# Optimization experiments

Measured on AMD Instinct MI355X. Metric: run time of the kernel, lower is better.

## Reference

```python
import jax, jax.numpy as jnp
import numpy as np

B, LC, LP = 8, 1024, 512
D, H, F, V, NL = 512, 8, 2048, 70, 4
MAXLEN = 2048
HD = D // H
EPS = 1e-5


def setup_inputs() -> dict:
    key = jax.random.key(0)
    ks = iter(jax.random.split(key, 64))
    s = lambda *sh: jax.random.normal(next(ks), sh, jnp.float32) * 0.02
    inp = {}
    inp['cds'] = jax.random.randint(next(ks), (B, LC), 0, V)
    inp['enc_prot'] = jax.random.normal(next(ks), (B, LP, D), jnp.float32)
    causal = jnp.tril(jnp.ones((LC, LC), jnp.int32))
    inp['cds_mask'] = jnp.broadcast_to(causal[None, None], (B, 1, LC, LC))
    inp['prot_mask'] = jnp.ones((B, 1, 1, LP), jnp.int32)
    inp['tok_emb'] = s(V, D)
    inp['pos_emb'] = s(MAXLEN, D)
    for p in ['sa', 'ca']:
        for m in ['q', 'k', 'v', 'o']:
            inp[f'{p}_w{m}'] = s(NL, D, D)
            inp[f'{p}_b{m}'] = jnp.zeros((NL, D), jnp.float32)
    inp['ff_w1'] = s(NL, D, F)
    inp['ff_b1'] = jnp.zeros((NL, F), jnp.float32)
    inp['ff_w2'] = s(NL, F, D)
    inp['ff_b2'] = jnp.zeros((NL, D), jnp.float32)
    for i in [1, 2, 3]:
        inp[f'ln{i}_g'] = jnp.ones((NL, D), jnp.float32)
        inp[f'ln{i}_b'] = jnp.zeros((NL, D), jnp.float32)
    inp['fc_out_w'] = s(D, V)
    inp['fc_out_b'] = jnp.zeros((V,), jnp.float32)
    return inp


def layernorm(x, g, b):
    mu = jnp.mean(x, -1, keepdims=True)
    var = jnp.var(x, -1, keepdims=True)
    return (x - mu) * jax.lax.rsqrt(var + EPS) * g + b


def mha(q_in, k_in, v_in, wq, bq, wk, bk, wv, bv, wo, bo, mask):
    b, lq, _ = q_in.shape
    lk = k_in.shape[1]
    q = (q_in @ wq + bq).reshape(b, lq, H, HD).transpose(0, 2, 1, 3)
    k = (k_in @ wk + bk).reshape(b, lk, H, HD).transpose(0, 2, 1, 3)
    v = (v_in @ wv + bv).reshape(b, lk, H, HD).transpose(0, 2, 1, 3)
    scores = jnp.einsum('bhqd,bhkd->bhqk', q, k) / jnp.sqrt(jnp.float32(HD))
    scores = jnp.where(mask == 0, -jnp.inf, scores)
    attn = jax.nn.softmax(scores, axis=-1)
    out = jnp.einsum('bhqk,bhkd->bhqd', attn, v)
    out = out.transpose(0, 2, 1, 3).reshape(b, lq, D)
    return out @ wo + bo, attn


def reference(cds, enc_prot, cds_mask, prot_mask, tok_emb, pos_emb,
              sa_wq, sa_bq, sa_wk, sa_bk, sa_wv, sa_bv, sa_wo, sa_bo,
              ca_wq, ca_bq, ca_wk, ca_bk, ca_wv, ca_bv, ca_wo, ca_bo,
              ff_w1, ff_b1, ff_w2, ff_b2,
              ln1_g, ln1_b, ln2_g, ln2_b, ln3_g, ln3_b,
              fc_out_w, fc_out_b):
    lc = cds.shape[1]
    x = tok_emb[cds] * jnp.sqrt(jnp.float32(D)) + pos_emb[:lc][None]
    attn = None
    for i in range(NL):
        sa, _ = mha(x, x, x, sa_wq[i], sa_bq[i], sa_wk[i], sa_bk[i],
                    sa_wv[i], sa_bv[i], sa_wo[i], sa_bo[i], cds_mask)
        x = layernorm(x + sa, ln1_g[i], ln1_b[i])
        ca, attn = mha(x, enc_prot, enc_prot, ca_wq[i], ca_bq[i], ca_wk[i], ca_bk[i],
                       ca_wv[i], ca_bv[i], ca_wo[i], ca_bo[i], prot_mask)
        x = layernorm(x + ca, ln2_g[i], ln2_b[i])
        ff = jax.nn.relu(x @ ff_w1[i] + ff_b1[i]) @ ff_w2[i] + ff_b2[i]
        x = layernorm(x + ff, ln3_g[i], ln3_b[i])
    logits = x @ fc_out_w + fc_out_b
    return logits, attn
```

## Files before the change

### kernel.cpp

```cpp
#include <hip/hip_runtime.h>

typedef __attribute__((ext_vector_type(8))) short bf16x8;
typedef __attribute__((ext_vector_type(4))) short bf16x4;
typedef __attribute__((ext_vector_type(4))) float f32x4;

#define D_MODEL 512
#define N_HEADS 8
#define HEAD_DIM 64
#define SEQ_C 1024
#define SEQ_P 512
#define BATCH 8
#define FFDIM 2048
#define VOCAB 70
#define NLAYER 4
#define MQ (BATCH*SEQ_C)
#define MKV (BATCH*SEQ_P)
#define KSTR 72

__device__ __forceinline__ short f2bs(float f) {
  union { float f; unsigned u; } v; v.f = f;
  unsigned r = (v.u + 0x7FFFu + ((v.u >> 16) & 1u)) >> 16;
  return (short)r;
}

__device__ __forceinline__ void gl_lds16(const void* g, void* l) {
  __builtin_amdgcn_global_load_lds(
      (const __attribute__((address_space(1))) void*)g,
      (__attribute__((address_space(3))) void*)l, 16, 0, 0);
}

__global__ __launch_bounds__(256)
void embed_kernel(const int* __restrict__ cds, const float* __restrict__ tok,
                  const float* __restrict__ pos, float* __restrict__ x,
                  short* __restrict__ xb) {
  int idx = blockIdx.x * 256 + threadIdx.x;
  int row = idx >> 9, c = idx & 511;
  int l = row & (SEQ_C - 1);
  int t = cds[row];
  float v = tok[t * D_MODEL + c] * 22.627416997969522f + pos[l * D_MODEL + c];
  x[idx] = v;
  xb[idx] = f2bs(v);
}

__global__ __launch_bounds__(256)
void cvtf2b_kernel(const float* __restrict__ in, short* __restrict__ out) {
  int i = (blockIdx.x * 256 + threadIdx.x) * 4;
  float4 v = *(const float4*)(in + i);
  bf16x4 o;
  o[0] = f2bs(v.x); o[1] = f2bs(v.y); o[2] = f2bs(v.z); o[3] = f2bs(v.w);
  *(bf16x4*)(out + i) = o;
}

struct WtArgs {
  const float* src[8];
  short* dst[8];
  size_t ldz[8];
  int row_off[8];
};

__global__ __launch_bounds__(256)
void wtrans8_kernel(WtArgs a) {
  __shared__ float T[32][33];
  int z = blockIdx.z;
  int job = z >> 2, layer = z & 3;
  const float* W = a.src[job] + (size_t)layer * D_MODEL * D_MODEL;
  short* Wt = a.dst[job] + (size_t)layer * a.ldz[job];
  int row_off = a.row_off[job];
  int n0 = blockIdx.x * 32, k0 = blockIdx.y * 32;
  int r = threadIdx.x >> 3, c4 = (threadIdx.x & 7) * 4;
  float4 v = *(const float4*)(W + (size_t)(k0 + r) * D_MODEL + n0 + c4);
  T[c4 + 0][r] = v.x; T[c4 + 1][r] = v.y; T[c4 + 2][r] = v.z; T[c4 + 3][r] = v.w;
  __syncthreads();
  bf16x4 o;
  o[0] = f2bs(T[r][c4 + 0]); o[1] = f2bs(T[r][c4 + 1]);
  o[2] = f2bs(T[r][c4 + 2]); o[3] = f2bs(T[r][c4 + 3]);
  *(bf16x4*)&Wt[(size_t)(row_off + n0 + r) * D_MODEL + k0 + c4] = o;
}

__global__ __launch_bounds__(256)
void wtrans_kernel(const float* __restrict__ W, short* __restrict__ Wt,
                   int K, int N, size_t dst_ldz) {
  __shared__ float T[32][33];
  size_t lo_s = (size_t)blockIdx.z * K * N;
  size_t lo_d = (size_t)blockIdx.z * dst_ldz;
  int n0 = blockIdx.x * 32, k0 = blockIdx.y * 32;
  int r = threadIdx.x >> 3, c4 = (threadIdx.x & 7) * 4;
  float4 v = *(const float4*)(W + lo_s + (size_t)(k0 + r) * N + n0 + c4);
  T[c4 + 0][r] = v.x; T[c4 + 1][r] = v.y; T[c4 + 2][r] = v.z; T[c4 + 3][r] = v.w;
  __syncthreads();
  bf16x4 o;
  o[0] = f2bs(T[r][c4 + 0]); o[1] = f2bs(T[r][c4 + 1]);
  o[2] = f2bs(T[r][c4 + 2]); o[3] = f2bs(T[r][c4 + 3]);
  *(bf16x4*)&Wt[lo_d + (size_t)(n0 + r) * K + k0 + c4] = o;
}

__global__ __launch_bounds__(256)
void logits_wt_kernel(const float* __restrict__ w, short* __restrict__ wt) {
  int idx = blockIdx.x * 256 + threadIdx.x;
  int r = idx >> 9, c = idx & 511;
  wt[idx] = (r < VOCAB) ? f2bs(w[c * VOCAB + r]) : (short)0;
}

template<int ACT, int OMODE, int MT>
__global__ __launch_bounds__(256)
void gemm_mfma(const short* __restrict__ Ab, const short* __restrict__ Wt,
               const float* __restrict__ b0, const float* __restrict__ b1,
               const float* __restrict__ b2,
               float* __restrict__ Cf, short* __restrict__ Cb,
               int N, int K, int ldc, size_t segstride) {
  constexpr int MREP = MT / 32;
  __shared__ __align__(16) short As[2][MT * 32];
  __shared__ __align__(16) short Bs[2][4096];
  int tid = threadIdx.x, lane = tid & 63, w = tid >> 6;
  int quad = lane >> 4, ln = lane & 15;
  int row0 = blockIdx.x * MT, col0 = blockIdx.y * 128;
  int q0 = tid, q1 = tid + 256;
  const short* a0 = Ab + (size_t)(row0 + (q0 >> 2)) * K + (q0 & 3) * 8;
  const short* a1 = Ab + (size_t)(row0 + (q1 >> 2)) * K + (q1 & 3) * 8;
  const short* w0 = Wt + (size_t)(col0 + (q0 >> 2)) * K + (q0 & 3) * 8;
  const short* w1 = Wt + (size_t)(col0 + (q1 >> 2)) * K + (q1 & 3) * 8;
  int wr = (w >> 1) * (MT / 2), wc = (w & 1) * 64;
  f32x4 acc[MREP][4];
  #pragma unroll
  for (int mb = 0; mb < MREP; mb++)
    #pragma unroll
    for (int nb = 0; nb < 4; nb++) acc[mb][nb] = (f32x4){0.f, 0.f, 0.f, 0.f};

  int nt = K >> 5;
#define STG(ko, buf) do { \
    gl_lds16(a0 + (ko), &As[buf][w * 512]); \
    if (MT == 128) gl_lds16(a1 + (ko), &As[buf][MT * 16 + w * 512]); \
    gl_lds16(w0 + (ko), &Bs[buf][w * 512]); \
    gl_lds16(w1 + (ko), &Bs[buf][2048 + w * 512]); } while (0)

  STG(0, 0);
  __syncthreads();
  for (int t = 0; t < nt; t++) {
    int cur = t & 1;
    if (t + 1 < nt) STG((t + 1) << 5, cur ^ 1);
    bf16x8 af[MREP], bfr[4];
    #pragma unroll
    for (int i = 0; i < MREP; i++)
      af[i] = *(const bf16x8*)&As[cur][(wr + i * 16 + ln) * 32 + quad * 8];
    #pragma unroll
    for (int i = 0; i < 4; i++)
      bfr[i] = *(const bf16x8*)&Bs[cur][(wc + i * 16 + ln) * 32 + quad * 8];
    #pragma unroll
    for (int mb = 0; mb < MREP; mb++)
      #pragma unroll
      for (int nb = 0; nb < 4; nb++)
        acc[mb][nb] = __builtin_amdgcn_mfma_f32_16x16x32_bf16(
            af[mb], bfr[nb], acc[mb][nb], 0, 0, 0);
    __syncthreads();
  }
#undef STG

  int colb = col0 + wc;
  const float* bp = b0;
  if (OMODE == 2) {
    int seg = colb >> 9;
    bp = (seg == 0) ? b0 : (seg == 1) ? b1 : b2;
  }
  float bv[4];
  #pragma unroll
  for (int nb = 0; nb < 4; nb++) {
    int col = colb + nb * 16 + ln;
    if (OMODE == 3)      bv[nb] = (col < ldc) ? bp[col] : 0.f;
    else if (OMODE == 2) bv[nb] = bp[col & 511];
    else                 bv[nb] = bp[col];
  }
  size_t segoff = (OMODE == 2) ? (size_t)(colb >> 9) * segstride : 0;
  #pragma unroll
  for (int mb = 0; mb < MREP; mb++)
    #pragma unroll
    for (int i = 0; i < 4; i++) {
      size_t r = (size_t)(row0 + wr + mb * 16 + quad * 4 + i);
      #pragma unroll
      for (int nb = 0; nb < 4; nb++) {
        int col = colb + nb * 16 + ln;
        float v = acc[mb][nb][i] + bv[nb];
        if (ACT) v = fmaxf(v, 0.f);
        if (OMODE == 0)      Cf[r * ldc + col] = v;
        else if (OMODE == 1) Cb[r * ldc + col] = f2bs(v);
        else if (OMODE == 2) Cb[segoff + r * 512 + (col & 511)] = f2bs(v);
        else if (col < ldc)  Cf[r * ldc + col] = v;
      }
    }
}

template<bool CAUSAL, bool SAVE_ML>
__global__ __launch_bounds__(256)
void flash_mfma(const short* __restrict__ Q, const short* __restrict__ K,
                const short* __restrict__ V, short* __restrict__ O,
                float* __restrict__ m_out, float* __restrict__ l_out,
                int LQ, int LK) {
  __shared__ short Ks[64 * KSTR];
  __shared__ short Vt[64 * KSTR];
  __shared__ short Ps[4 * 16 * KSTR];
  const float scale = 0.125f;
  int qt = CAUSAL ? ((int)gridDim.x - 1 - (int)blockIdx.x) : (int)blockIdx.x;
  int bh = blockIdx.y;
  int b = bh >> 3, h = bh & 7;
  int tid = threadIdx.x, lane = tid & 63, w = tid >> 6;
  int quad = lane >> 4, ln = lane & 15;

  const short* qp = Q + (size_t)(b * LQ + qt * 64 + w * 16 + ln) * D_MODEL + h * HEAD_DIM;
  bf16x8 qf[2];
  qf[0] = *(const bf16x8*)(qp + quad * 8);
  qf[1] = *(const bf16x8*)(qp + 32 + quad * 8);

  int qrow = qt * 64 + w * 16 + ln;
  float m_q = -__builtin_inff(), l_q = 0.f;
  f32x4 o_acc[4];
  #pragma unroll
  for (int nb = 0; nb < 4; nb++) o_acc[nb] = (f32x4){0.f, 0.f, 0.f, 0.f};

  const short* Kb = K + (size_t)(b * LK) * D_MODEL + h * HEAD_DIM;
  const short* Vb = V + (size_t)(b * LK) * D_MODEL + h * HEAD_DIM;
  int sr = tid >> 2, sc = (tid & 3) * 16;
  int br4 = (tid >> 4) * 4, bc4 = (tid & 15) * 4;

  bf16x8 krA, krB;
  bf16x4 vr0, vr1, vr2, vr3;

#define LOADKV(KT) do { \
    const short* kg_ = Kb + (size_t)((KT) * 64 + sr) * D_MODEL + sc; \
    krA = *(const bf16x8*)kg_; krB = *(const bf16x8*)(kg_ + 8); \
    const short* vg_ = Vb + (size_t)((KT) * 64 + br4) * D_MODEL + bc4; \
    vr0 = *(const bf16x4*)(vg_); \
    vr1 = *(const bf16x4*)(vg_ + D_MODEL); \
    vr2 = *(const bf16x4*)(vg_ + 2 * D_MODEL); \
    vr3 = *(const bf16x4*)(vg_ + 3 * D_MODEL); } while (0)

  LOADKV(0);
  int nkt = CAUSAL ? (qt + 1) : (LK >> 6);
  for (int kt = 0; kt < nkt; kt++) {
    __syncthreads();
    *(bf16x8*)&Ks[sr * KSTR + sc]     = krA;
    *(bf16x8*)&Ks[sr * KSTR + sc + 8] = krB;
    #pragma unroll
    for (int jj = 0; jj < 4; jj++) {
      bf16x4 t;
      t[0] = vr0[jj]; t[1] = vr1[jj]; t[2] = vr2[jj]; t[3] = vr3[jj];
      *(bf16x4*)&Vt[(bc4 + jj) * KSTR + br4] = t;
    }
    if (kt + 1 < nkt) LOADKV(kt + 1);
    __syncthreads();

    f32x4 st[4];
    __builtin_amdgcn_s_setprio(1);
    #pragma unroll
    for (int nb = 0; nb < 4; nb++) {
      st[nb] = (f32x4){0.f, 0.f, 0.f, 0.f};
      bf16x8 kf0 = *(const bf16x8*)&Ks[(nb * 16 + ln) * KSTR + quad * 8];
      bf16x8 kf1 = *(const bf16x8*)&Ks[(nb * 16 + ln) * KSTR + 32 + quad * 8];
      st[nb] = __builtin_amdgcn_mfma_f32_16x16x32_bf16(kf0, qf[0], st[nb], 0, 0, 0);
      st[nb] = __builtin_amdgcn_mfma_f32_16x16x32_bf16(kf1, qf[1], st[nb], 0, 0, 0);
    }
    __builtin_amdgcn_s_setprio(0);

    float sv[4][4];
    float mt = -__builtin_inff();
    #pragma unroll
    for (int nb = 0; nb < 4; nb++)
      #pragma unroll
      for (int i = 0; i < 4; i++) {
        float v = st[nb][i] * scale;
        if (CAUSAL && (kt * 64 + nb * 16 + quad * 4 + i) > qrow) v = -__builtin_inff();
        sv[nb][i] = v;
        mt = fmaxf(mt, v);
      }
    mt = fmaxf(mt, __shfl_xor(mt, 16));
    mt = fmaxf(mt, __shfl_xor(mt, 32));
    float mnew = fmaxf(m_q, mt);
    float alpha = __expf(m_q - mnew);
    float rs = 0.f;
    bf16x4 pk[4];
    #pragma unroll
    for (int nb = 0; nb < 4; nb++)
      #pragma unroll
      for (int i = 0; i < 4; i++) {
        float p = __expf(sv[nb][i] - mnew);
        rs += p;
        pk[nb][i] = f2bs(p);
      }
    rs += __shfl_xor(rs, 16);
    rs += __shfl_xor(rs, 32);
    l_q = l_q * alpha + rs;
    m_q = mnew;

    #pragma unroll
    for (int nb = 0; nb < 4; nb++)
      *(bf16x4*)&Ps[w * 16 * KSTR + ln * KSTR + nb * 16 + quad * 4] = pk[nb];
    #pragma unroll
    for (int i = 0; i < 4; i++) {
      float ai = __shfl(alpha, ((lane >> 4) << 2) + i);
      #pragma unroll
      for (int nb = 0; nb < 4; nb++) o_acc[nb][i] *= ai;
    }

    __builtin_amdgcn_s_setprio(1);
    #pragma unroll
    for (int kb = 0; kb < 2; kb++) {
      bf16x8 pf = *(const bf16x8*)&Ps[w * 16 * KSTR + ln * KSTR + kb * 32 + quad * 8];
      #pragma unroll
      for (int nb = 0; nb < 4; nb++) {
        bf16x8 vf = *(const bf16x8*)&Vt[(nb * 16 + ln) * KSTR + kb * 32 + quad * 8];
        o_acc[nb] = __builtin_amdgcn_mfma_f32_16x16x32_bf16(pf, vf, o_acc[nb], 0, 0, 0);
      }
    }
    __builtin_amdgcn_s_setprio(0);
  }
#undef LOADKV

  short* Ob = O + (size_t)(b * LQ + qt * 64 + w * 16 + quad * 4) * D_MODEL + h * HEAD_DIM;
  #pragma unroll
  for (int i = 0; i < 4; i++) {
    float li = __shfl(l_q, ((lane >> 4) << 2) + i);
    float inv = 1.f / li;
    #pragma unroll
    for (int nb = 0; nb < 4; nb++)
      Ob[(size_t)i * D_MODEL + nb * 16 + ln] = f2bs(o_acc[nb][i] * inv);
  }
  if (SAVE_ML && lane < 16) {
    int r = bh * LQ + qt * 64 + w * 16 + lane;
    m_out[r] = m_q;
    l_out[r] = l_q;
  }
}

__global__ __launch_bounds__(256)
void attn_prob_mfma(const short* __restrict__ Q, const short* __restrict__ K,
                    const float* __restrict__ m_in, const float* __restrict__ l_in,
                    float* __restrict__ out) {
  __shared__ short Ks[64 * KSTR];
  const float scale = 0.125f;
  int qt = blockIdx.x, bh = blockIdx.y;
  int b = bh >> 3, h = bh & 7;
  int tid = threadIdx.x, lane = tid & 63, w = tid >> 6;
  int quad = lane >> 4, ln = lane & 15;
  const short* qp = Q + (size_t)(b * SEQ_C + qt * 64 + w * 16 + ln) * D_MODEL + h * HEAD_DIM;
  bf16x8 qf[2];
  qf[0] = *(const bf16x8*)(qp + quad * 8);
  qf[1] = *(const bf16x8*)(qp + 32 + quad * 8);
  float m_r[4], il[4];
  #pragma unroll
  for (int i = 0; i < 4; i++) {
    int r = bh * SEQ_C + qt * 64 + w * 16 + quad * 4 + i;
    m_r[i] = m_in[r]; il[i] = 1.f / l_in[r];
  }
  const short* Kb = K + (size_t)(b * SEQ_P) * D_MODEL + h * HEAD_DIM;
  int sr = tid >> 2, sc = (tid & 3) * 16;
  bf16x8 krA, krB;
  {
    const short* kg = Kb + (size_t)sr * D_MODEL + sc;
    krA = *(const bf16x8*)kg; krB = *(const bf16x8*)(kg + 8);
  }
  for (int kt = 0; kt < (SEQ_P >> 6); kt++) {
    __syncthreads();
    *(bf16x8*)&Ks[sr * KSTR + sc]     = krA;
    *(bf16x8*)&Ks[sr * KSTR + sc + 8] = krB;
    if (kt + 1 < (SEQ_P >> 6)) {
      const short* kg = Kb + (size_t)((kt + 1) * 64 + sr) * D_MODEL + sc;
      krA = *(const bf16x8*)kg; krB = *(const bf16x8*)(kg + 8);
    }
    __syncthreads();
    #pragma unroll
    for (int nb = 0; nb < 4; nb++) {
      f32x4 s = (f32x4){0.f, 0.f, 0.f, 0.f};
      bf16x8 kf0 = *(const bf16x8*)&Ks[(nb * 16 + ln) * KSTR + quad * 8];
      bf16x8 kf1 = *(const bf16x8*)&Ks[(nb * 16 + ln) * KSTR + 32 + quad * 8];
      s = __builtin_amdgcn_mfma_f32_16x16x32_bf16(qf[0], kf0, s, 0, 0, 0);
      s = __builtin_amdgcn_mfma_f32_16x16x32_bf16(qf[1], kf1, s, 0, 0, 0);
      #pragma unroll
      for (int i = 0; i < 4; i++) {
        size_t off = ((size_t)bh * SEQ_C + qt * 64 + w * 16 + quad * 4 + i) * SEQ_P
                   + kt * 64 + nb * 16 + ln;
        out[off] = __expf(s[i] * scale - m_r[i]) * il[i];
      }
    }
  }
}

__global__ __launch_bounds__(256)
void add_ln_kernel(float* __restrict__ x, const float* __restrict__ y,
                   const float* __restrict__ g, const float* __restrict__ b,
                   short* __restrict__ xb) {
  int row = blockIdx.x * 4 + (threadIdx.x >> 6);
  int lane = threadIdx.x & 63;
  float* xr = x + (size_t)row * D_MODEL;
  short* xbr = xb + (size_t)row * D_MODEL;
  const float* yr = y + (size_t)row * D_MODEL;
  float v[8]; float s = 0.f, sq = 0.f;
  #pragma unroll
  for (int i = 0; i < 8; i++) {
    int c = lane + 64 * i;
    float t = xr[c] + yr[c];
    v[i] = t; s += t; sq += t * t;
  }
  #pragma unroll
  for (int m = 1; m < 64; m <<= 1) { s += __shfl_xor(s, m); sq += __shfl_xor(sq, m); }
  float mu = s * (1.0f / 512.0f);
  float var = sq * (1.0f / 512.0f) - mu * mu;
  float rstd = rsqrtf(var + 1e-5f);
  #pragma unroll
  for (int i = 0; i < 8; i++) {
    int c = lane + 64 * i;
    float r = (v[i] - mu) * rstd * g[c] + b[c];
    xr[c] = r;
    xbr[c] = f2bs(r);
  }
}

extern "C" void kernel_launch(void* const* d_in, const int* in_sizes, int n_in,
                              void* d_out, int out_size, void* d_ws, size_t ws_size,
                              hipStream_t stream) {
  (void)in_sizes; (void)n_in; (void)out_size; (void)ws_size;
  const int*   cds      = (const int*)d_in[0];
  const float* enc_prot = (const float*)d_in[1];
  const float* tok_emb  = (const float*)d_in[4];
  const float* pos_emb  = (const float*)d_in[5];
  const float* sa_wq = (const float*)d_in[6];  const float* sa_bq = (const float*)d_in[7];
  const float* sa_wk = (const float*)d_in[8];  const float* sa_bk = (const float*)d_in[9];
  const float* sa_wv = (const float*)d_in[10]; const float* sa_bv = (const float*)d_in[11];
  const float* sa_wo = (const float*)d_in[12]; const float* sa_bo = (const float*)d_in[13];
  const float* ca_wq = (const float*)d_in[14]; const float* ca_bq = (const float*)d_in[15];
  const float* ca_wk = (const float*)d_in[16]; const float* ca_bk = (const float*)d_in[17];
  const float* ca_wv = (const float*)d_in[18]; const float* ca_bv = (const float*)d_in[19];
  const float* ca_wo = (const float*)d_in[20]; const float* ca_bo = (const float*)d_in[21];
  const float* ff_w1 = (const float*)d_in[22]; const float* ff_b1 = (const float*)d_in[23];
  const float* ff_w2 = (const float*)d_in[24]; const float* ff_b2 = (const float*)d_in[25];
  const float* ln1_g = (const float*)d_in[26]; const float* ln1_b = (const float*)d_in[27];
  const float* ln2_g = (const float*)d_in[28]; const float* ln2_b = (const float*)d_in[29];
  const float* ln3_g = (const float*)d_in[30]; const float* ln3_b = (const float*)d_in[31];
  const float* fcw   = (const float*)d_in[32]; const float* fcb   = (const float*)d_in[33];

  float* x    = (float*)d_ws;
  float* y    = x + (size_t)MQ * D_MODEL;
  float* mbuf = y + (size_t)MQ * D_MODEL;
  float* lbuf = mbuf + (size_t)BATCH * N_HEADS * SEQ_C;
  short* xb   = (short*)(lbuf + (size_t)BATCH * N_HEADS * SEQ_C);
  short* qb   = xb + (size_t)MQ * D_MODEL;
  short* kb   = qb + (size_t)MQ * D_MODEL;
  short* vb   = kb + (size_t)MQ * D_MODEL;
  short* ctxb = vb + (size_t)MQ * D_MODEL;
  short* hb   = qb;
  short* encb = ctxb + (size_t)MQ * D_MODEL;
  short* wtb  = encb + (size_t)MKV * D_MODEL;
  short* wts  = wtb + (size_t)128 * D_MODEL;
  const size_t WSZ = (size_t)NLAYER * D_MODEL * D_MODEL;
  short* w_saqkv = wts;
  short* w_sao   = w_saqkv + 3 * WSZ;
  short* w_caq   = w_sao + WSZ;
  short* w_cakv  = w_caq + WSZ;
  short* w_cao   = w_cakv + 2 * WSZ;
  short* w_ff1   = w_cao + WSZ;
  short* w_ff2   = w_ff1 + (size_t)NLAYER * D_MODEL * FFDIM;

  float* logits = (float*)d_out;
  float* attn   = logits + (size_t)MQ * VOCAB;

  const size_t SEG = (size_t)MQ * D_MODEL;
  const size_t L1536 = (size_t)1536 * 512, L1024 = (size_t)1024 * 512, L512 = (size_t)512 * 512;

  embed_kernel<<<MQ * D_MODEL / 256, 256, 0, stream>>>(cds, tok_emb, pos_emb, x, xb);
  cvtf2b_kernel<<<(size_t)MKV * D_MODEL / 1024, 256, 0, stream>>>(enc_prot, encb);
  logits_wt_kernel<<<128 * D_MODEL / 256, 256, 0, stream>>>(fcw, wtb);
  {
    WtArgs a;
    a.src[0] = sa_wq; a.dst[0] = w_saqkv; a.ldz[0] = L1536; a.row_off[0] = 0;
    a.src[1] = sa_wk; a.dst[1] = w_saqkv; a.ldz[1] = L1536; a.row_off[1] = 512;
    a.src[2] = sa_wv; a.dst[2] = w_saqkv; a.ldz[2] = L1536; a.row_off[2] = 1024;
    a.src[3] = sa_wo; a.dst[3] = w_sao;   a.ldz[3] = L512;  a.row_off[3] = 0;
    a.src[4] = ca_wq; a.dst[4] = w_caq;   a.ldz[4] = L512;  a.row_off[4] = 0;
    a.src[5] = ca_wk; a.dst[5] = w_cakv;  a.ldz[5] = L1024; a.row_off[5] = 0;
    a.src[6] = ca_wv; a.dst[6] = w_cakv;  a.ldz[6] = L1024; a.row_off[6] = 512;
    a.src[7] = ca_wo; a.dst[7] = w_cao;   a.ldz[7] = L512;  a.row_off[7] = 0;
    wtrans8_kernel<<<dim3(16, 16, 8 * NLAYER), 256, 0, stream>>>(a);
  }
  wtrans_kernel<<<dim3(FFDIM / 32, D_MODEL / 32, NLAYER), 256, 0, stream>>>(
      ff_w1, w_ff1, D_MODEL, FFDIM, (size_t)FFDIM * 512);
  wtrans_kernel<<<dim3(D_MODEL / 32, FFDIM / 32, NLAYER), 256, 0, stream>>>(
      ff_w2, w_ff2, FFDIM, D_MODEL, (size_t)512 * FFDIM);

  dim3 gqkv(MQ / 128, 1536 / 128);
  dim3 gq64(MQ / 64, D_MODEL / 128);
  dim3 gkv64(MKV / 64, 1024 / 128);
  dim3 gf1(MQ / 128, FFDIM / 128);
  dim3 glg(MQ / 64, 1);
  dim3 ga(SEQ_C / 64, BATCH * N_HEADS);

  for (int i = 0; i < NLAYER; i++) {
    size_t wo_ = (size_t)i * D_MODEL * D_MODEL, bo_ = (size_t)i * D_MODEL;
    size_t wf_ = (size_t)i * D_MODEL * FFDIM;
    gemm_mfma<0,2,128><<<gqkv, 256, 0, stream>>>(xb, w_saqkv + (size_t)i * L1536,
        sa_bq + bo_, sa_bk + bo_, sa_bv + bo_, nullptr, qb, 1536, 512, 512, SEG);
    flash_mfma<true,  false><<<ga, 256, 0, stream>>>(qb, kb, vb, ctxb, nullptr, nullptr, SEQ_C, SEQ_C);
    gemm_mfma<0,0,64><<<gq64, 256, 0, stream>>>(ctxb, w_sao + wo_,
        sa_bo + bo_, nullptr, nullptr, y, nullptr, 512, 512, 512, 0);
    add_ln_kernel<<<MQ / 4, 256, 0, stream>>>(x, y, ln1_g + bo_, ln1_b + bo_, xb);
    gemm_mfma<0,1,64><<<gq64, 256, 0, stream>>>(xb, w_caq + wo_,
        ca_bq + bo_, nullptr, nullptr, nullptr, qb, 512, 512, 512, 0);
    gemm_mfma<0,2,64><<<gkv64, 256, 0, stream>>>(encb, w_cakv + (size_t)i * L1024,
        ca_bk + bo_, ca_bv + bo_, nullptr, nullptr, kb, 1024, 512, 512, SEG);
    if (i == NLAYER - 1) {
      flash_mfma<false, true><<<ga, 256, 0, stream>>>(qb, kb, vb, ctxb, mbuf, lbuf, SEQ_C, SEQ_P);
      attn_prob_mfma<<<ga, 256, 0, stream>>>(qb, kb, mbuf, lbuf, attn);
    } else {
      flash_mfma<false, false><<<ga, 256, 0, stream>>>(qb, kb, vb, ctxb, nullptr, nullptr, SEQ_C, SEQ_P);
    }
    gemm_mfma<0,0,64><<<gq64, 256, 0, stream>>>(ctxb, w_cao + wo_,
        ca_bo + bo_, nullptr, nullptr, y, nullptr, 512, 512, 512, 0);
    add_ln_kernel<<<MQ / 4, 256, 0, stream>>>(x, y, ln2_g + bo_, ln2_b + bo_, xb);
    gemm_mfma<1,1,128><<<gf1, 256, 0, stream>>>(xb, w_ff1 + wf_,
        ff_b1 + (size_t)i * FFDIM, nullptr, nullptr, nullptr, hb, FFDIM, 512, FFDIM, 0);
    gemm_mfma<0,0,64><<<gq64, 256, 0, stream>>>(hb, w_ff2 + wf_,
        ff_b2 + bo_, nullptr, nullptr, y, nullptr, 512, FFDIM, 512, 0);
    add_ln_kernel<<<MQ / 4, 256, 0, stream>>>(x, y, ln3_g + bo_, ln3_b + bo_, xb);
  }
  gemm_mfma<0,3,64><<<glg, 256, 0, stream>>>(xb, wtb,
      fcb, nullptr, nullptr, logits, nullptr, 128, 512, VOCAB, 0);
}
```

Measured before the change: 1.300 ms.

## Double-buffer K/V in flash attention with 128-row query tiles and vectorize add+LN

The flash attention kernel now runs 512 threads (8 waves) per block and covers 128 query rows, so each K/V tile is shared by twice as many rows. K/V shared memory is double-buffered, which removes one barrier per iteration and overlaps the next tile's store with compute. The add+layernorm kernel uses float2 and bf16x2 accesses. In exchange there are half as many attention blocks, more shared memory per block, and causal blocks where some waves do masked work.

```diff
diff --git a/kernel.cpp b/kernel.cpp
--- a/kernel.cpp
+++ b/kernel.cpp
@@ -2,6 +2,7 @@
 
 typedef __attribute__((ext_vector_type(8))) short bf16x8;
 typedef __attribute__((ext_vector_type(4))) short bf16x4;
+typedef __attribute__((ext_vector_type(2))) short bf16x2;
 typedef __attribute__((ext_vector_type(4))) float f32x4;
 
 #define D_MODEL 512
@@ -189,14 +190,14 @@
 }
 
 template<bool CAUSAL, bool SAVE_ML>
-__global__ __launch_bounds__(256)
+__global__ __launch_bounds__(512)
 void flash_mfma(const short* __restrict__ Q, const short* __restrict__ K,
                 const short* __restrict__ V, short* __restrict__ O,
                 float* __restrict__ m_out, float* __restrict__ l_out,
                 int LQ, int LK) {
-  __shared__ short Ks[64 * KSTR];
-  __shared__ short Vt[64 * KSTR];
-  __shared__ short Ps[4 * 16 * KSTR];
+  __shared__ short Ks[2][64 * KSTR];
+  __shared__ short Vt[2][64 * KSTR];
+  __shared__ short Ps[8 * 16 * KSTR];
   const float scale = 0.125f;
   int qt = CAUSAL ? ((int)gridDim.x - 1 - (int)blockIdx.x) : (int)blockIdx.x;
   int bh = blockIdx.y;
@@ -204,12 +205,12 @@
   int tid = threadIdx.x, lane = tid & 63, w = tid >> 6;
   int quad = lane >> 4, ln = lane & 15;
 
-  const short* qp = Q + (size_t)(b * LQ + qt * 64 + w * 16 + ln) * D_MODEL + h * HEAD_DIM;
+  const short* qp = Q + (size_t)(b * LQ + qt * 128 + w * 16 + ln) * D_MODEL + h * HEAD_DIM;
   bf16x8 qf[2];
   qf[0] = *(const bf16x8*)(qp + quad * 8);
   qf[1] = *(const bf16x8*)(qp + 32 + quad * 8);
 
-  int qrow = qt * 64 + w * 16 + ln;
+  int qrow = qt * 128 + w * 16 + ln;
   float m_q = -__builtin_inff(), l_q = 0.f;
   f32x4 o_acc[4];
   #pragma unroll
@@ -217,43 +218,51 @@
 
   const short* Kb = K + (size_t)(b * LK) * D_MODEL + h * HEAD_DIM;
   const short* Vb = V + (size_t)(b * LK) * D_MODEL + h * HEAD_DIM;
-  int sr = tid >> 2, sc = (tid & 3) * 16;
+  int sr = tid >> 3, sc = (tid & 7) * 8;
   int br4 = (tid >> 4) * 4, bc4 = (tid & 15) * 4;
-
-  bf16x8 krA, krB;
+  bool vst = tid < 256;
+
+  bf16x8 kr;
   bf16x4 vr0, vr1, vr2, vr3;
 
 #define LOADKV(KT) do { \
-    const short* kg_ = Kb + (size_t)((KT) * 64 + sr) * D_MODEL + sc; \
-    krA = *(const bf16x8*)kg_; krB = *(const bf16x8*)(kg_ + 8); \
-    const short* vg_ = Vb + (size_t)((KT) * 64 + br4) * D_MODEL + bc4; \
-    vr0 = *(const bf16x4*)(vg_); \
-    vr1 = *(const bf16x4*)(vg_ + D_MODEL); \
-    vr2 = *(const bf16x4*)(vg_ + 2 * D_MODEL); \
-    vr3 = *(const bf16x4*)(vg_ + 3 * D_MODEL); } while (0)
-
+    kr = *(const bf16x8*)(Kb + (size_t)((KT) * 64 + sr) * D_MODEL + sc); \
+    if (vst) { \
+      const short* vg_ = Vb + (size_t)((KT) * 64 + br4) * D_MODEL + bc4; \
+      vr0 = *(const bf16x4*)(vg_); \
+      vr1 = *(const bf16x4*)(vg_ + D_MODEL); \
+      vr2 = *(const bf16x4*)(vg_ + 2 * D_MODEL); \
+      vr3 = *(const bf16x4*)(vg_ + 3 * D_MODEL); } } while (0)
+
+#define STORKV(BUF) do { \
+    *(bf16x8*)&Ks[BUF][sr * KSTR + sc] = kr; \
+    if (vst) { \
+      _Pragma("unroll") \
+      for (int jj = 0; jj < 4; jj++) { \
+        bf16x4 t_; \
+        t_[0] = vr0[jj]; t_[1] = vr1[jj]; t_[2] = vr2[jj]; t_[3] = vr3[jj]; \
+        *(bf16x4*)&Vt[BUF][(bc4 + jj) * KSTR + br4] = t_; } } } while (0)
+
+  int nkt = CAUSAL ? (2 * qt + 2) : (LK >> 6);
   LOADKV(0);
-  int nkt = CAUSAL ? (qt + 1) : (LK >> 6);
+  STORKV(0);
+  if (nkt > 1) LOADKV(1);
+  __syncthreads();
+
   for (int kt = 0; kt < nkt; kt++) {
-    __syncthreads();
-    *(bf16x8*)&Ks[sr * KSTR + sc]     = krA;
-    *(bf16x8*)&Ks[sr * KSTR + sc + 8] = krB;
-    #pragma unroll
-    for (int jj = 0; jj < 4; jj++) {
-      bf16x4 t;
-      t[0] = vr0[jj]; t[1] = vr1[jj]; t[2] = vr2[jj]; t[3] = vr3[jj];
-      *(bf16x4*)&Vt[(bc4 + jj) * KSTR + br4] = t;
-    }
-    if (kt + 1 < nkt) LOADKV(kt + 1);
-    __syncthreads();
+    int cur = kt & 1;
+    if (kt + 1 < nkt) {
+      STORKV(cur ^ 1);
+      if (kt + 2 < nkt) LOADKV(kt + 2);
+    }
 
     f32x4 st[4];
     __builtin_amdgcn_s_setprio(1);
     #pragma unroll
     for (int nb = 0; nb < 4; nb++) {
       st[nb] = (f32x4){0.f, 0.f, 0.f, 0.f};
-      bf16x8 kf0 = *(const bf16x8*)&Ks[(nb * 16 + ln) * KSTR + quad * 8];
-      bf16x8 kf1 = *(const bf16x8*)&Ks[(nb * 16 + ln) * KSTR + 32 + quad * 8];
+      bf16x8 kf0 = *(const bf16x8*)&Ks[cur][(nb * 16 + ln) * KSTR + quad * 8];
+      bf16x8 kf1 = *(const bf16x8*)&Ks[cur][(nb * 16 + ln) * KSTR + 32 + quad * 8];
       st[nb] = __builtin_amdgcn_mfma_f32_16x16x32_bf16(kf0, qf[0], st[nb], 0, 0, 0);
       st[nb] = __builtin_amdgcn_mfma_f32_16x16x32_bf16(kf1, qf[1], st[nb], 0, 0, 0);
     }
@@ -305,15 +314,17 @@
       bf16x8 pf = *(const bf16x8*)&Ps[w * 16 * KSTR + ln * KSTR + kb * 32 + quad * 8];
       #pragma unroll
       for (int nb = 0; nb < 4; nb++) {
-        bf16x8 vf = *(const bf16x8*)&Vt[(nb * 16 + ln) * KSTR + kb * 32 + quad * 8];
+        bf16x8 vf = *(const bf16x8*)&Vt[cur][(nb * 16 + ln) * KSTR + kb * 32 + quad * 8];
         o_acc[nb] = __builtin_amdgcn_mfma_f32_16x16x32_bf16(pf, vf, o_acc[nb], 0, 0, 0);
       }
     }
     __builtin_amdgcn_s_setprio(0);
+    __syncthreads();
   }
 #undef LOADKV
-
-  short* Ob = O + (size_t)(b * LQ + qt * 64 + w * 16 + quad * 4) * D_MODEL + h * HEAD_DIM;
+#undef STORKV
+
+  short* Ob = O + (size_t)(b * LQ + qt * 128 + w * 16 + quad * 4) * D_MODEL + h * HEAD_DIM;
   #pragma unroll
   for (int i = 0; i < 4; i++) {
     float li = __shfl(l_q, ((lane >> 4) << 2) + i);
@@ -323,7 +334,7 @@
       Ob[(size_t)i * D_MODEL + nb * 16 + ln] = f2bs(o_acc[nb][i] * inv);
   }
   if (SAVE_ML && lane < 16) {
-    int r = bh * LQ + qt * 64 + w * 16 + lane;
+    int r = bh * LQ + qt * 128 + w * 16 + lane;
     m_out[r] = m_q;
     l_out[r] = l_q;
   }
@@ -388,15 +399,16 @@
                    short* __restrict__ xb) {
   int row = blockIdx.x * 4 + (threadIdx.x >> 6);
   int lane = threadIdx.x & 63;
-  float* xr = x + (size_t)row * D_MODEL;
-  short* xbr = xb + (size_t)row * D_MODEL;
-  const float* yr = y + (size_t)row * D_MODEL;
-  float v[8]; float s = 0.f, sq = 0.f;
-  #pragma unroll
-  for (int i = 0; i < 8; i++) {
+  float2* xr = (float2*)(x + (size_t)row * D_MODEL);
+  bf16x2* xbr = (bf16x2*)(xb + (size_t)row * D_MODEL);
+  const float2* yr = (const float2*)(y + (size_t)row * D_MODEL);
+  float2 v[4]; float s = 0.f, sq = 0.f;
+  #pragma unroll
+  for (int i = 0; i < 4; i++) {
     int c = lane + 64 * i;
-    float t = xr[c] + yr[c];
-    v[i] = t; s += t; sq += t * t;
+    float2 a = xr[c], d = yr[c];
+    a.x += d.x; a.y += d.y;
+    v[i] = a; s += a.x + a.y; sq += a.x * a.x + a.y * a.y;
   }
   #pragma unroll
   for (int m = 1; m < 64; m <<= 1) { s += __shfl_xor(s, m); sq += __shfl_xor(sq, m); }
@@ -404,11 +416,13 @@
   float var = sq * (1.0f / 512.0f) - mu * mu;
   float rstd = rsqrtf(var + 1e-5f);
   #pragma unroll
-  for (int i = 0; i < 8; i++) {
+  for (int i = 0; i < 4; i++) {
     int c = lane + 64 * i;
-    float r = (v[i] - mu) * rstd * g[c] + b[c];
-    xr[c] = r;
-    xbr[c] = f2bs(r);
+    float r0 = (v[i].x - mu) * rstd * g[2 * c] + b[2 * c];
+    float r1 = (v[i].y - mu) * rstd * g[2 * c + 1] + b[2 * c + 1];
+    xr[c] = make_float2(r0, r1);
+    bf16x2 o; o[0] = f2bs(r0); o[1] = f2bs(r1);
+    xbr[c] = o;
   }
 }
 
@@ -488,14 +502,15 @@
   dim3 gkv64(MKV / 64, 1024 / 128);
   dim3 gf1(MQ / 128, FFDIM / 128);
   dim3 glg(MQ / 64, 1);
-  dim3 ga(SEQ_C / 64, BATCH * N_HEADS);
+  dim3 ga(SEQ_C / 128, BATCH * N_HEADS);
+  dim3 gap(SEQ_C / 64, BATCH * N_HEADS);
 
   for (int i = 0; i < NLAYER; i++) {
     size_t wo_ = (size_t)i * D_MODEL * D_MODEL, bo_ = (size_t)i * D_MODEL;
     size_t wf_ = (size_t)i * D_MODEL * FFDIM;
     gemm_mfma<0,2,128><<<gqkv, 256, 0, stream>>>(xb, w_saqkv + (size_t)i * L1536,
         sa_bq + bo_, sa_bk + bo_, sa_bv + bo_, nullptr, qb, 1536, 512, 512, SEG);
-    flash_mfma<true,  false><<<ga, 256, 0, stream>>>(qb, kb, vb, ctxb, nullptr, nullptr, SEQ_C, SEQ_C);
+    flash_mfma<true,  false><<<ga, 512, 0, stream>>>(qb, kb, vb, ctxb, nullptr, nullptr, SEQ_C, SEQ_C);
     gemm_mfma<0,0,64><<<gq64, 256, 0, stream>>>(ctxb, w_sao + wo_,
         sa_bo + bo_, nullptr, nullptr, y, nullptr, 512, 512, 512, 0);
     add_ln_kernel<<<MQ / 4, 256, 0, stream>>>(x, y, ln1_g + bo_, ln1_b + bo_, xb);
@@ -504,10 +519,10 @@
     gemm_mfma<0,2,64><<<gkv64, 256, 0, stream>>>(encb, w_cakv + (size_t)i * L1024,
         ca_bk + bo_, ca_bv + bo_, nullptr, nullptr, kb, 1024, 512, 512, SEG);
     if (i == NLAYER - 1) {
-      flash_mfma<false, true><<<ga, 256, 0, stream>>>(qb, kb, vb, ctxb, mbuf, lbuf, SEQ_C, SEQ_P);
-      attn_prob_mfma<<<ga, 256, 0, stream>>>(qb, kb, mbuf, lbuf, attn);
+      flash_mfma<false, true><<<ga, 512, 0, stream>>>(qb, kb, vb, ctxb, mbuf, lbuf, SEQ_C, SEQ_P);
+      attn_prob_mfma<<<gap, 256, 0, stream>>>(qb, kb, mbuf, lbuf, attn);
     } else {
-      flash_mfma<false, false><<<ga, 256, 0, stream>>>(qb, kb, vb, ctxb, nullptr, nullptr, SEQ_C, SEQ_P);
+      flash_mfma<false, false><<<ga, 512, 0, stream>>>(qb, kb, vb, ctxb, nullptr, nullptr, SEQ_C, SEQ_P);
     }
     gemm_mfma<0,0,64><<<gq64, 256, 0, stream>>>(ctxb, w_cao + wo_,
         ca_bo + bo_, nullptr, nullptr, y, nullptr, 512, 512, 512, 0);
```

Measured after the change: 1.279 ms. About the same (-1.7%).
